# Kernel tuning notes

Measured on AMD Instinct MI355X. Metric: run time of the kernel, lower is better.

Reference implementation:

```python
import jax, jax.numpy as jnp
import numpy as np

B, N, E, H = 2, 4096, 1024, 16
HD = E // H                      # head_dim = 64
R = 8                            # LoRA rank
LORA_SCALE = 16.0 / R            # alpha / r = 2.0
BUCKET_SIZES = (256, 64, 16)


def setup_inputs() -> dict:
    key = jax.random.key(0)
    ks = jax.random.split(key, 24)
    inp = {"x": jax.random.normal(ks[0], (B, N, E), jnp.float32)}
    inp["wb_coarse"] = jax.random.randint(ks[1], (B, N), 0, 16)
    inp["wb_mid"] = jax.random.randint(ks[2], (B, N), 0, 64)
    inp["wb_fine"] = jax.random.randint(ks[3], (B, N), 0, 256)
    i = 4
    for name in ("q", "k", "v", "o"):
        inp[f"W{name}"] = jax.random.normal(ks[i], (E, E), jnp.float32) / np.sqrt(E); i += 1
        inp[f"b{name}"] = jax.random.normal(ks[i], (E,), jnp.float32) * 0.01; i += 1
        inp[f"A{name}"] = jax.random.normal(ks[i], (R, E), jnp.float32) / np.sqrt(E); i += 1
        inp[f"B{name}"] = jax.random.normal(ks[i], (E, R), jnp.float32) * 0.01; i += 1
    return inp


def _lora(x, W, b, A, Bm):
    # F.linear(x, W, b) + scale * x @ A.T @ B.T   (dropout=0 in eval)
    return x @ W.T + b + LORA_SCALE * ((x @ A.T) @ Bm.T)


def _chunked_attn(q, k, v, bidx, C):
    # q,k,v: [BH, N, D]; bidx: [BH, N] int; C: chunk size (divides N)
    BH, Nn, D = q.shape
    sidx = jnp.argsort(bidx, axis=1)
    uidx = jnp.argsort(sidx, axis=1)
    g = lambda t, i: jnp.take_along_axis(t, i[..., None], axis=1)
    qs, ks_, vs = g(q, sidx), g(k, sidx), g(v, sidx)
    nc = Nn // C
    qs = qs.reshape(BH, nc, C, D)
    ks_ = ks_.reshape(BH, nc, C, D)
    vs = vs.reshape(BH, nc, C, D)
    # previous chunk (look-back of one chunk); chunk 0 has no previous -> masked
    k_prev = jnp.concatenate([jnp.zeros_like(ks_[:, :1]), ks_[:, :-1]], axis=1)
    v_prev = jnp.concatenate([jnp.zeros_like(vs[:, :1]), vs[:, :-1]], axis=1)
    k_cat = jnp.concatenate([k_prev, ks_], axis=2)   # [BH, nc, 2C, D]
    v_cat = jnp.concatenate([v_prev, vs], axis=2)
    scores = jnp.einsum('bncd,bnkd->bnck', qs, k_cat) / jnp.sqrt(jnp.asarray(D, qs.dtype))
    # mask look-back keys for chunk 0 (torch path attends only within chunk 0)
    chunk_ids = jnp.arange(nc)[:, None, None]        # [nc,1,1]
    key_pos = jnp.arange(2 * C)[None, None, :]       # [1,1,2C]
    neg = jnp.finfo(scores.dtype).min
    scores = jnp.where((chunk_ids == 0) & (key_pos < C), neg, scores)
    attn = jax.nn.softmax(scores, axis=-1)
    out = jnp.einsum('bnck,bnkd->bncd', attn, v_cat).reshape(BH, Nn, D)
    return jnp.take_along_axis(out, uidx[..., None], axis=1)


def reference(x, wb_coarse, wb_mid, wb_fine,
              Wq, bq, Aq, Bq, Wk, bk, Ak, Bk,
              Wv, bv, Av, Bv, Wo, bo, Ao, Bo):
    q = _lora(x, Wq, bq, Aq, Bq)
    k = _lora(x, Wk, bk, Ak, Bk)
    v = _lora(x, Wv, bv, Av, Bv)
    to_heads = lambda t: t.reshape(B, N, H, HD).transpose(0, 2, 1, 3).reshape(B * H, N, HD)
    qh, kh, vh = to_heads(q), to_heads(k), to_heads(v)
    expand = lambda w: jnp.broadcast_to(w[:, None, :], (B, H, N)).reshape(B * H, N)
    wbs = (expand(wb_coarse), expand(wb_mid), expand(wb_fine))
    outs = (_chunked_attn(qh, kh, vh, wbs[0], BUCKET_SIZES[0])
            + _chunked_attn(qh, kh, vh, wbs[1], BUCKET_SIZES[1])
            + _chunked_attn(qh, kh, vh, wbs[2], BUCKET_SIZES[2])) / 3.0
    outs = outs.reshape(B, H, N, HD).transpose(0, 2, 1, 3).reshape(B, N, E)
    return _lora(outs, Wo, bo, Ao, Bo)
```

## Files before the change

kernel.cpp:

```cpp
#include <hip/hip_runtime.h>
#include <cstdint>
#include <cstddef>

#define BDIM 2
#define NTOK 4096
#define EDIM 1024
#define HEADS 16
#define HDIM 64
#define MROWS (BDIM * NTOK)

typedef unsigned short u16;
typedef __attribute__((ext_vector_type(8))) short bf16x8;
typedef __attribute__((ext_vector_type(8))) unsigned short u16x8;
typedef __attribute__((ext_vector_type(4))) float f32x4;

#define MFMA(a, b, c) __builtin_amdgcn_mfma_f32_16x16x32_bf16(a, b, c, 0, 0, 0)
#define BAR() asm volatile("s_barrier" ::: "memory")
#define SETPRIO(p) __builtin_amdgcn_s_setprio(p)

__device__ inline void split2(float x, u16& h, u16& l) {
    union { float f; unsigned u; } a;
    a.f = x;
    unsigned uh = a.u + 0x7fff + ((a.u >> 16) & 1);
    h = (u16)(uh >> 16);
// ... 34 lines not shown
    int o = idx >> 10, i = idx & 1023;
    float sum = 0.f;
#pragma unroll
    for (int r = 0; r < 8; ++r) sum += Bm[o * 8 + r] * A[r * 1024 + i];
    float w = W[idx] + 2.0f * sum;
    u16 h, l;
    split2(w, h, l);
    dh[idx] = h; dl[idx] = l;
}

__global__ __launch_bounds__(256) void split_kernel(
    const float* __restrict__ src, u16* __restrict__ dh, u16* __restrict__ dl)
{
    int idx = blockIdx.x * 256 + threadIdx.x;
    float4 v = ((const float4*)src)[idx];
    ushort4 h, l;
    split2(v.x, h.x, l.x);
    split2(v.y, h.y, l.y);
    split2(v.z, h.z, l.z);
    split2(v.w, h.w, l.w);
    ((ushort4*)dh)[idx] = h;
    ((ushort4*)dl)[idx] = l;
}

__global__ __launch_bounds__(256) void sort3_kernel(
    const int* __restrict__ w0, const int* __restrict__ w1,
    const int* __restrict__ w2, int* __restrict__ sidx)
{
    __shared__ int sb[NTOK];
    __shared__ int cnt[32][256];
    __shared__ int gb[256];
    const int* srcs[3] = {w0, w1, w2};
    int t = threadIdx.x;
    const int* w = srcs[blockIdx.y] + blockIdx.x * NTOK;
    int* outp = sidx + ((int)blockIdx.y * BDIM + (int)blockIdx.x) * NTOK;

    for (int i = t; i < NTOK; i += 256) sb[i] = w[i];
    for (int i = t; i < 32 * 256; i += 256) ((int*)cnt)[i] = 0;
    __syncthreads();

    int g = t >> 3;
#pragma unroll
    for (int e = 0; e < 16; ++e)
        atomicAdd(&cnt[g][sb[g * 128 + (t & 7) + 8 * e]], 1);
    __syncthreads();

    int run = 0;
#pragma unroll
    for (int gg = 0; gg < 32; ++gg) {
        int c = cnt[gg][t];
        cnt[gg][t] = run;
        run += c;
    }
    gb[t] = run;
    __syncthreads();
    if (t == 0) {
        int acc = 0;
        for (int v = 0; v < 256; ++v) { int c = gb[v]; gb[v] = acc; acc += c; }
    }
    __syncthreads();
    for (int i = t; i < 32 * 256; i += 256) {
        int v = i & 255, gg = i >> 8;
        cnt[gg][v] += gb[v];
    }
    __syncthreads();

    if (t < 32) {
        int base = t * 128;
        for (int e = 0; e < 128; ++e) {
            int v = sb[base + e];
            int p = cnt[t][v]++;
            outp[p] = base + e;
        }
    }
}

__global__ __launch_bounds__(512, 2) void gemm_qk_kernel(
    const u16* __restrict__ Xh, const u16* __restrict__ Xl,
    const u16* __restrict__ Wh, const u16* __restrict__ Wl,
    const float* __restrict__ bq, const float* __restrict__ bk,
    u16* __restrict__ qh, u16* __restrict__ ql,
    u16* __restrict__ kh, u16* __restrict__ kl)
{
    __shared__ __align__(16) unsigned char smem[131072];
    u16* lds = (u16*)smem;
    const int PA_h = 0, PA_l = 8192, PB_h = 16384, PB_l = 24576;

    int t = threadIdx.x;
    int lane = t & 63, wave = t >> 6;
    int bid = blockIdx.x;
    int wg = (bid & 7) * 32 + (bid >> 3);
    int bx = wg & 7, by = wg >> 3;
    int m0 = by * 256, n0 = bx * 256;

    int lrow = lane & 15, lq = lane >> 4;
    size_t aoff = (size_t)(m0 + wave * 32 + lrow) * EDIM + lq * 8;
    size_t boff = (size_t)(n0 + wave * 32 + lrow) * EDIM + lq * 8;
    int slabA = wave * 2;
    int sA0 = (wave >> 2) * 8;
    int sB0 = (wave & 3) * 4;
    f32x4 acc[8][4] = {};

    {
        u16* b0 = lds;
        GLL(Xh + aoff,             b0 + PA_h + (slabA + 0) * 512);
        GLL(Xh + aoff + 16 * EDIM, b0 + PA_h + (slabA + 1) * 512);
        GLL(Xl + aoff,             b0 + PA_l + (slabA + 0) * 512);
        GLL(Xl + aoff + 16 * EDIM, b0 + PA_l + (slabA + 1) * 512);
        GLL(Wh + boff,             b0 + PB_h + (slabA + 0) * 512);
        GLL(Wh + boff + 16 * EDIM, b0 + PB_h + (slabA + 1) * 512);
        GLL(Wl + boff,             b0 + PB_l + (slabA + 0) * 512);
        GLL(Wl + boff + 16 * EDIM, b0 + PB_l + (slabA + 1) * 512);
    }
    asm volatile("s_waitcnt vmcnt(0)" ::: "memory");
    BAR();

    for (int t32 = 0; t32 < 32; ++t32) {
        u16* rb   = lds + (t32 & 1) * 32768;
        u16* wbuf = lds + ((t32 + 1) & 1) * 32768;
        bool pf = (t32 + 1) < 32;
        int kn = (t32 + 1) * 32;
        bf16x8 bhf[4], blf[4];
#pragma unroll
        for (int p = 0; p < 4; ++p) {
            if (p == 0) {
#pragma unroll
                for (int j = 0; j < 4; ++j) {
                    bhf[j] = *(const bf16x8*)(rb + PB_h + (sB0 + j) * 512 + lane * 8);
                    blf[j] = *(const bf16x8*)(rb + PB_l + (sB0 + j) * 512 + lane * 8);
                }
            }
            bf16x8 a0h = *(const bf16x8*)(rb + PA_h + (sA0 + 2 * p)     * 512 + lane * 8);
            bf16x8 a0l = *(const bf16x8*)(rb + PA_l + (sA0 + 2 * p)     * 512 + lane * 8);
            bf16x8 a1h = *(const bf16x8*)(rb + PA_h + (sA0 + 2 * p + 1) * 512 + lane * 8);
            bf16x8 a1l = *(const bf16x8*)(rb + PA_l + (sA0 + 2 * p + 1) * 512 + lane * 8);
            if (pf) {
                if (p == 0) {
                    GLL(Xh + aoff + kn,             wbuf + PA_h + (slabA + 0) * 512);
                    GLL(Xh + aoff + kn + 16 * EDIM, wbuf + PA_h + (slabA + 1) * 512);
                    GLL(Xl + aoff + kn,             wbuf + PA_l + (slabA + 0) * 512);
                } else if (p == 1) {
                    GLL(Xl + aoff + kn + 16 * EDIM, wbuf + PA_l + (slabA + 1) * 512);
                    GLL(Wh + boff + kn,             wbuf + PB_h + (slabA + 0) * 512);
                    GLL(Wh + boff + kn + 16 * EDIM, wbuf + PB_h + (slabA + 1) * 512);
                } else if (p == 2) {
                    GLL(Wl + boff + kn,             wbuf + PB_l + (slabA + 0) * 512);
                    GLL(Wl + boff + kn + 16 * EDIM, wbuf + PB_l + (slabA + 1) * 512);
                }
            }
            BAR();
            SETPRIO(1);
#pragma unroll
            for (int j = 0; j < 4; ++j) {
                acc[2 * p][j]     = MFMA(a0h, bhf[j], acc[2 * p][j]);
                acc[2 * p][j]     = MFMA(a0h, blf[j], acc[2 * p][j]);
                acc[2 * p][j]     = MFMA(a0l, bhf[j], acc[2 * p][j]);
                acc[2 * p + 1][j] = MFMA(a1h, bhf[j], acc[2 * p + 1][j]);
                acc[2 * p + 1][j] = MFMA(a1h, blf[j], acc[2 * p + 1][j]);
                acc[2 * p + 1][j] = MFMA(a1l, bhf[j], acc[2 * p + 1][j]);
            }
            SETPRIO(0);
            if (p == 3) asm volatile("s_waitcnt vmcnt(0)" ::: "memory");
            BAR();
        }
    }

    int proj = n0 >> 10;
    const float* bias = proj ? bk : bq;
    u16* oh = proj ? kh : qh;
    u16* ol = proj ? kl : ql;
    int wm = (wave >> 2) * 128, wn = (wave & 3) * 64;
    int q4 = lane >> 4, l16 = lane & 15;
    int cb = (n0 & 1023) + wn;
    float bj[4];
#pragma unroll
    for (int j = 0; j < 4; ++j) bj[j] = bias[cb + j * 16 + l16];
    float* repw = (float*)smem + wave * 2176;
    int r8 = lane >> 3, c8 = lane & 7;
#pragma unroll
    for (int g = 0; g < 4; ++g) {
#pragma unroll
        for (int ii = 0; ii < 2; ++ii)
#pragma unroll
            for (int j = 0; j < 4; ++j)
#pragma unroll
                for (int r = 0; r < 4; ++r)
                    repw[(ii * 16 + q4 * 4 + r) * 68 + j * 16 + l16] =
                        acc[g * 2 + ii][j][r] + bj[j];
#pragma unroll
        for (int rg = 0; rg < 4; ++rg) {
            int lr = rg * 8 + r8;
            float4 f0 = *(float4*)(repw + lr * 68 + c8 * 8);
            float4 f1 = *(float4*)(repw + lr * 68 + c8 * 8 + 4);
            float fa[8] = {f0.x, f0.y, f0.z, f0.w, f1.x, f1.y, f1.z, f1.w};
            size_t off = (size_t)(m0 + wm + g * 32 + lr) * EDIM + cb + c8 * 8;
            u16x8 hv, lv;
#pragma unroll
            for (int e = 0; e < 8; ++e) {
                float v = fa[e];
                if (proj == 0) v *= 0.125f;
                u16 hh, ll;
                split2(v, hh, ll);
                hv[e] = hh; lv[e] = ll;
            }
            *(u16x8*)(oh + off) = hv;
            *(u16x8*)(ol + off) = lv;
        }
    }
}

__global__ __launch_bounds__(512, 2) void gemm_v_kernel(
    const u16* __restrict__ Xh, const u16* __restrict__ Wv,
    const float* __restrict__ bv, u16* __restrict__ vh)
{
    __shared__ __align__(16) unsigned char smem[73728];
    u16* lds = (u16*)smem;

    int t = threadIdx.x;
    int lane = t & 63, wave = t >> 6;
    int bid = blockIdx.x;
    int wg = (bid & 7) * 32 + (bid >> 3);
    int bx = wg & 7, by = wg >> 3;
    int m0 = by * 256, nc0 = bx * 128;

    int lrow = lane & 15, lq = lane >> 4;
    size_t aoff = (size_t)(m0 + wave * 32 + lrow) * EDIM + lq * 8;
    size_t boff = (size_t)(nc0 + wave * 16 + lrow) * EDIM + lq * 8;
    int slabA = wave * 2;
    int sA0 = (wave >> 1) * 4;
    int sB0 = (wave & 1) * 4;
    f32x4 acc[4][4] = {};

#pragma unroll
    for (int tt = 0; tt < 2; ++tt) {
        u16* sb = lds + tt * 12288;
        int kk = tt * 32;
        GLL(Xh + aoff + kk,             sb + (slabA + 0) * 512);
        GLL(Xh + aoff + kk + 16 * EDIM, sb + (slabA + 1) * 512);
        GLL(Wv + boff + kk,             sb + 8192 + wave * 512);
    }
    asm volatile("s_waitcnt vmcnt(3)" ::: "memory");
    BAR();

    for (int t32 = 0; t32 < 32; ++t32) {
        u16* rb = lds + (t32 % 3) * 12288;
        u16* sb = lds + ((t32 + 2) % 3) * 12288;
        bool pf = (t32 + 2) < 32;
        int kn = (t32 + 2) * 32;

        bf16x8 bhf[4];
#pragma unroll
        for (int j = 0; j < 4; ++j)
            bhf[j] = *(const bf16x8*)(rb + 8192 + (sB0 + j) * 512 + lane * 8);
        bf16x8 a0 = *(const bf16x8*)(rb + (sA0 + 0) * 512 + lane * 8);
        bf16x8 a1 = *(const bf16x8*)(rb + (sA0 + 1) * 512 + lane * 8);
        if (pf) {
            GLL(Xh + aoff + kn,             sb + (slabA + 0) * 512);
            GLL(Xh + aoff + kn + 16 * EDIM, sb + (slabA + 1) * 512);
        }
        BAR();
        SETPRIO(1);
#pragma unroll
        for (int j = 0; j < 4; ++j) {
            acc[0][j] = MFMA(a0, bhf[j], acc[0][j]);
            acc[1][j] = MFMA(a1, bhf[j], acc[1][j]);
        }
        SETPRIO(0);
        BAR();

        bf16x8 a2 = *(const bf16x8*)(rb + (sA0 + 2) * 512 + lane * 8);
        bf16x8 a3 = *(const bf16x8*)(rb + (sA0 + 3) * 512 + lane * 8);
        if (pf) GLL(Wv + boff + kn, sb + 8192 + wave * 512);
        BAR();
        SETPRIO(1);
#pragma unroll
        for (int j = 0; j < 4; ++j) {
            acc[2][j] = MFMA(a2, bhf[j], acc[2][j]);
            acc[3][j] = MFMA(a3, bhf[j], acc[3][j]);
        }
        SETPRIO(0);
        if (pf) asm volatile("s_waitcnt vmcnt(3)" ::: "memory");
        else    asm volatile("s_waitcnt vmcnt(0)" ::: "memory");
        BAR();
    }

    int wm = (wave >> 1) * 64, wn = (wave & 1) * 64;
    int q4 = lane >> 4, l16 = lane & 15;
    int cb = nc0 + wn;
    float bj[4];
#pragma unroll
    for (int j = 0; j < 4; ++j) bj[j] = bv[cb + j * 16 + l16];
    float* repw = (float*)smem + wave * 2176;
    int r8 = lane >> 3, c8 = lane & 7;
#pragma unroll
    for (int g = 0; g < 2; ++g) {
#pragma unroll
        for (int ii = 0; ii < 2; ++ii)
#pragma unroll
            for (int j = 0; j < 4; ++j)
#pragma unroll
                for (int r = 0; r < 4; ++r)
                    repw[(ii * 16 + q4 * 4 + r) * 68 + j * 16 + l16] =
                        acc[g * 2 + ii][j][r] + bj[j];
#pragma unroll
        for (int rg = 0; rg < 4; ++rg) {
            int lr = rg * 8 + r8;
            float4 f0 = *(float4*)(repw + lr * 68 + c8 * 8);
            float4 f1 = *(float4*)(repw + lr * 68 + c8 * 8 + 4);
            float fa[8] = {f0.x, f0.y, f0.z, f0.w, f1.x, f1.y, f1.z, f1.w};
            size_t off = (size_t)(m0 + wm + g * 32 + lr) * EDIM + cb + c8 * 8;
            u16x8 hv;
#pragma unroll
            for (int e = 0; e < 8; ++e) hv[e] = bf16rne(fa[e]);
            *(u16x8*)(vh + off) = hv;
        }
    }
}

__global__ __launch_bounds__(512, 2) void gemm_o_kernel(
    const u16* __restrict__ Xh, const u16* __restrict__ Xl,
    const u16* __restrict__ Wh, const u16* __restrict__ Wl,
    const float* __restrict__ bias, float* __restrict__ Y)
{
    __shared__ __align__(16) unsigned char smem[147456];
    u16* lds = (u16*)smem;
    const int PA_h = 0, PA_l = 8192, PB_h = 16384, PB_l = 20480;

    int t = threadIdx.x;
    int lane = t & 63, wave = t >> 6;
    int bid = blockIdx.x;
    int wg = (bid & 7) * 32 + (bid >> 3);
    int bx = wg & 7, by = wg >> 3;
    int m0 = by * 256, n0 = bx * 128;

    int lrow = lane & 15, lq = lane >> 4;
    size_t aoff = (size_t)(m0 + wave * 32 + lrow) * EDIM + lq * 8;
    size_t boff = (size_t)(n0 + wave * 16 + lrow) * EDIM + lq * 8;
    int slabA = wave * 2;
    int sA0 = (wave >> 1) * 4;
    int sB0 = (wave & 1) * 4;
    f32x4 acc[4][4] = {};

#pragma unroll
    for (int tt = 0; tt < 2; ++tt) {
        u16* sb = lds + tt * 24576;
        int kk = tt * 32;
        GLL(Xh + aoff + kk,             sb + PA_h + (slabA + 0) * 512);
        GLL(Xh + aoff + kk + 16 * EDIM, sb + PA_h + (slabA + 1) * 512);
        GLL(Xl + aoff + kk,             sb + PA_l + (slabA + 0) * 512);
        GLL(Xl + aoff + kk + 16 * EDIM, sb + PA_l + (slabA + 1) * 512);
        GLL(Wh + boff + kk,             sb + PB_h + wave * 512);
        GLL(Wl + boff + kk,             sb + PB_l + wave * 512);
    }
    asm volatile("s_waitcnt vmcnt(6)" ::: "memory");
    BAR();

    for (int t32 = 0; t32 < 32; ++t32) {
        u16* rb = lds + (t32 % 3) * 24576;
        u16* sb = lds + ((t32 + 2) % 3) * 24576;
        bool pf = (t32 + 2) < 32;
        int kn = (t32 + 2) * 32;
        bf16x8 bhf[4], blf[4];
#pragma unroll
        for (int p = 0; p < 4; ++p) {
            if (p == 0) {
#pragma unroll
                for (int j = 0; j < 4; ++j) {
                    bhf[j] = *(const bf16x8*)(rb + PB_h + (sB0 + j) * 512 + lane * 8);
                    blf[j] = *(const bf16x8*)(rb + PB_l + (sB0 + j) * 512 + lane * 8);
                }
            }
            bf16x8 aph = *(const bf16x8*)(rb + PA_h + (sA0 + p) * 512 + lane * 8);
            bf16x8 apl = *(const bf16x8*)(rb + PA_l + (sA0 + p) * 512 + lane * 8);
            if (pf) {
                if (p == 0) {
                    GLL(Xh + aoff + kn,             sb + PA_h + (slabA + 0) * 512);
                    GLL(Xh + aoff + kn + 16 * EDIM, sb + PA_h + (slabA + 1) * 512);
                } else if (p == 1) {
                    GLL(Xl + aoff + kn,             sb + PA_l + (slabA + 0) * 512);
                    GLL(Xl + aoff + kn + 16 * EDIM, sb + PA_l + (slabA + 1) * 512);
                } else if (p == 2) {
                    GLL(Wh + boff + kn, sb + PB_h + wave * 512);
                    GLL(Wl + boff + kn, sb + PB_l + wave * 512);
                }
            }
            BAR();
            SETPRIO(1);
#pragma unroll
            for (int j = 0; j < 4; ++j) {
                acc[p][j] = MFMA(aph, bhf[j], acc[p][j]);
                acc[p][j] = MFMA(aph, blf[j], acc[p][j]);
                acc[p][j] = MFMA(apl, bhf[j], acc[p][j]);
            }
            SETPRIO(0);
            if (p == 3) {
                if (pf) asm volatile("s_waitcnt vmcnt(6)" ::: "memory");
                else    asm volatile("s_waitcnt vmcnt(0)" ::: "memory");
            }
            BAR();
        }
    }

    int wm = (wave >> 1) * 64, wn = (wave & 1) * 64;
    int col_in = lane & 15, rquad = lane >> 4;
#pragma unroll
    for (int j = 0; j < 4; ++j) {
        int col = n0 + wn + j * 16 + col_in;
        float bvv = bias[col];
#pragma unroll
        for (int i = 0; i < 4; ++i) {
            int mbase = m0 + wm + i * 16 + rquad * 4;
#pragma unroll
            for (int r = 0; r < 4; ++r)
                Y[(size_t)(mbase + r) * EDIM + col] = acc[i][j][r] + bvv;
        }
    }
}

template <int C>
__global__ __launch_bounds__(256, 3) void attn_mfma_kernel(
    const u16* __restrict__ Qh, const u16* __restrict__ Ql,
    const u16* __restrict__ Kh, const u16* __restrict__ Kl,
    const u16* __restrict__ Vh, const int* __restrict__ sidx,
    float* __restrict__ out)
{
    __shared__ u16 KfH[4096], KfL[4096];
    __shared__ u16 VL[64 * 72];
    __shared__ u16 PbH[4 * 16 * 56];

    int t = threadIdx.x;
    int lane = t & 63, wave = t >> 6;
    int quad = lane >> 4, l16 = lane & 15;
    int bh = blockIdx.y, b = bh >> 4, h = bh & 15;
    int p0 = blockIdx.x * 128;
    const int* sxb = sidx + b * NTOK;

    int ptile[2], ws_[2], we_[2];
    bf16x8 qhf[2][2], qlf[2][2];
#pragma unroll
    for (int tq = 0; tq < 2; ++tq) {
        ptile[tq] = p0 + wave * 32 + tq * 16;
        int c = ptile[tq] / C;
        ws_[tq] = (c > 0) ? (c - 1) * C : 0;
        we_[tq] = (c + 1) * C;
        int qrow = sxb[ptile[tq] + l16];
        size_t rb = (size_t)(b * NTOK + qrow) * EDIM + h * HDIM + quad * 8;
#pragma unroll
        for (int kk = 0; kk < 2; ++kk) {
            qhf[tq][kk] = *(const bf16x8*)(Qh + rb + kk * 32);
            qlf[tq][kk] = *(const bf16x8*)(Ql + rb + kk * 32);
        }
    }

    f32x4 oacc[2][4] = {};
    float lpart[2][4] = {};
    float mrun[2] = {-1e30f, -1e30f};

    int c0 = p0 / C, c1 = (p0 + 127) / C;
    int kmin = (c0 > 0) ? (c0 - 1) * C : 0;
    int kmax = (c1 + 1) * C;

    for (int ks = kmin; ks < kmax; ks += 64) {
        int nk = min(64, kmax - ks);
        __syncthreads();

        {
            int key16 = lane & 15, qd = lane >> 4;
            int tok = sxb[min(ks + wave * 16 + key16, NTOK - 1)];
            size_t rb = (size_t)(b * NTOK + tok) * EDIM + h * HDIM + qd * 8;
            GLL(Kh + rb,      KfH + (wave * 2 + 0) * 512);
            GLL(Kh + rb + 32, KfH + (wave * 2 + 1) * 512);
            GLL(Kl + rb,      KfL + (wave * 2 + 0) * 512);
            GLL(Kl + rb + 32, KfL + (wave * 2 + 1) * 512);
        }
#pragma unroll
        for (int it = 0; it < 2; ++it) {
            int c = it * 256 + t;
            int key = c & 63, dg = c >> 6;
            int tok = sxb[min(ks + key, NTOK - 1)];
            bf16x8 vv = *(const bf16x8*)(Vh + (size_t)(b * NTOK + tok) * EDIM + h * HDIM + dg * 8);
#pragma unroll
            for (int e = 0; e < 8; ++e)
                VL[(dg * 8 + e) * 72 + key] = (u16)vv[e];
        }
        __syncthreads();

        int jlo0 = max(ks, ws_[0]) - ks, jhi0 = min(ks + nk, we_[0]) - ks;
        int jlo1 = max(ks, ws_[1]) - ks, jhi1 = min(ks + nk, we_[1]) - ks;
        bool e0 = jlo0 < jhi0, e1 = jlo1 < jhi1;
        if (!e0 && !e1) continue;
        int glo = e0 ? (e1 ? min(jlo0, jlo1) : jlo0) : jlo1;
        int ghi = e0 ? (e1 ? max(jhi0, jhi1) : jhi0) : jhi1;

        for (int g0 = glo & ~31; g0 < ghi; g0 += 32) {
            int s0i = g0 >> 4;
            int s1i = min(s0i + 1, 3);
            bf16x8 kh0[2], kl0[2], kh1[2], kl1[2];
#pragma unroll
            for (int kk = 0; kk < 2; ++kk) {
                kh0[kk] = *(const bf16x8*)(KfH + ((s0i * 2 + kk) * 64 + lane) * 8);
                kl0[kk] = *(const bf16x8*)(KfL + ((s0i * 2 + kk) * 64 + lane) * 8);
                kh1[kk] = *(const bf16x8*)(KfH + ((s1i * 2 + kk) * 64 + lane) * 8);
                kl1[kk] = *(const bf16x8*)(KfL + ((s1i * 2 + kk) * 64 + lane) * 8);
            }
#pragma unroll
            for (int tq = 0; tq < 2; ++tq) {
                int jl = tq ? jlo1 : jlo0, jh = tq ? jhi1 : jhi0;
                bool v0 = (g0 >= jl) && (g0 < jh);
                bool v1 = (g0 + 16 >= jl) && (g0 + 16 < jh);
                if (!v0 && !v1) continue;
                f32x4 sa = {0.f, 0.f, 0.f, 0.f}, sb2 = {0.f, 0.f, 0.f, 0.f};
                if (v0) {
                    sa = MFMA(qhf[tq][0], kh0[0], sa);
                    sa = MFMA(qhf[tq][0], kl0[0], sa);
                    sa = MFMA(qlf[tq][0], kh0[0], sa);
                    sa = MFMA(qhf[tq][1], kh0[1], sa);
                    sa = MFMA(qhf[tq][1], kl0[1], sa);
                    sa = MFMA(qlf[tq][1], kh0[1], sa);
                }
                if (v1) {
                    sb2 = MFMA(qhf[tq][0], kh1[0], sb2);
                    sb2 = MFMA(qhf[tq][0], kl1[0], sb2);
                    sb2 = MFMA(qlf[tq][0], kh1[0], sb2);
                    sb2 = MFMA(qhf[tq][1], kh1[1], sb2);
                    sb2 = MFMA(qhf[tq][1], kl1[1], sb2);
                    sb2 = MFMA(qlf[tq][1], kh1[1], sb2);
                }
                float smax = -1e30f;
                if (v0) smax = fmaxf(smax, fmaxf(fmaxf(sa[0], sa[1]), fmaxf(sa[2], sa[3])));
                if (v1) smax = fmaxf(smax, fmaxf(fmaxf(sb2[0], sb2[1]), fmaxf(sb2[2], sb2[3])));
                smax = fmaxf(smax, __shfl_xor(smax, 1));
                smax = fmaxf(smax, __shfl_xor(smax, 2));
                smax = fmaxf(smax, __shfl_xor(smax, 4));
                smax = fmaxf(smax, __shfl_xor(smax, 8));
                float mold = mrun[tq];
                float mnew = fmaxf(mold, smax);
                mrun[tq] = mnew;
                float alpha = __expf(mold - mnew);
#pragma unroll
                for (int r = 0; r < 4; ++r) lpart[tq][r] *= alpha;
#pragma unroll
                for (int dt = 0; dt < 4; ++dt) {
                    oacc[tq][dt][0] *= alpha; oacc[tq][dt][1] *= alpha;
                    oacc[tq][dt][2] *= alpha; oacc[tq][dt][3] *= alpha;
                }
                u16* pbh = PbH + wave * 896;
#pragma unroll
                for (int r = 0; r < 4; ++r) {
                    float pa = v0 ? __expf(sa[r] - mnew) : 0.f;
                    float pb = v1 ? __expf(sb2[r] - mnew) : 0.f;
                    lpart[tq][r] += pa + pb;
                    pbh[(quad * 4 + r) * 56 + l16] = bf16rne(pa);
                    pbh[(quad * 4 + r) * 56 + 16 + l16] = bf16rne(pb);
                }
                bf16x8 ph = *(const bf16x8*)(pbh + l16 * 56 + quad * 8);
                int kh2 = g0 >> 5;
#pragma unroll
                for (int dt = 0; dt < 4; ++dt) {
                    bf16x8 vv = *(const bf16x8*)(VL + (dt * 16 + l16) * 72 + kh2 * 32 + quad * 8);
                    oacc[tq][dt] = MFMA(ph, vv, oacc[tq][dt]);
                }
            }
        }
    }

#pragma unroll
    for (int tq = 0; tq < 2; ++tq) {
        float inv[4];
#pragma unroll
        for (int r = 0; r < 4; ++r) {
            float v = lpart[tq][r];
            v += __shfl_xor(v, 1);
            v += __shfl_xor(v, 2);
            v += __shfl_xor(v, 4);
            v += __shfl_xor(v, 8);
            inv[r] = 1.0f / (3.0f * v);
        }
#pragma unroll
        for (int r = 0; r < 4; ++r) {
            int tok = sxb[ptile[tq] + quad * 4 + r];
            float* op = out + (size_t)(b * NTOK + tok) * EDIM + h * HDIM + l16;
#pragma unroll
            for (int dt = 0; dt < 4; ++dt)
                op[dt * 16] += oacc[tq][dt][r] * inv[r];
        }
    }
}

extern "C" void kernel_launch(void* const* d_in, const int* in_sizes, int n_in,
                              void* d_out, int out_size, void* d_ws, size_t ws_size,
                              hipStream_t stream)
{
    const float* x   = (const float*)d_in[0];
    const int*   wbc = (const int*)d_in[1];
    const int*   wbm = (const int*)d_in[2];
    const int*   wbf = (const int*)d_in[3];
    const float* Wq = (const float*)d_in[4],  *bq = (const float*)d_in[5];
    const float* Aq = (const float*)d_in[6],  *Bq = (const float*)d_in[7];
    const float* Wk = (const float*)d_in[8],  *bk = (const float*)d_in[9];
    const float* Ak = (const float*)d_in[10], *Bk = (const float*)d_in[11];
    const float* Wv = (const float*)d_in[12], *bv = (const float*)d_in[13];
    const float* Av = (const float*)d_in[14], *Bv = (const float*)d_in[15];
    const float* Wo = (const float*)d_in[16], *bo = (const float*)d_in[17];
    const float* Ao = (const float*)d_in[18], *Bo = (const float*)d_in[19];

    const size_t EE  = (size_t)EDIM * EDIM;
    const size_t BNE = (size_t)MROWS * EDIM;

    char* wsb = (char*)d_ws;
    float* ab = (float*)wsb;                        wsb += BNE * 4;
    u16* xh = (u16*)wsb;                            wsb += BNE * 2;
    u16* xl = (u16*)wsb;                            wsb += BNE * 2;
    u16* qh = (u16*)wsb;                            wsb += BNE * 2;
    u16* ql = (u16*)wsb;                            wsb += BNE * 2;
    u16* kh = (u16*)wsb;                            wsb += BNE * 2;
    u16* kl = (u16*)wsb;                            wsb += BNE * 2;
    u16* vh = (u16*)wsb;                            wsb += BNE * 2;
    u16* wh_all = (u16*)wsb;                        wsb += 3 * EE * 2;
    u16* wl_all = (u16*)wsb;                        wsb += 3 * EE * 2;
    u16* woh = (u16*)wsb;                           wsb += EE * 2;
    u16* wol = (u16*)wsb;                           wsb += EE * 2;
    int* sidx = (int*)wsb;                          wsb += 3 * BDIM * NTOK * 4;

    hipMemsetAsync(ab, 0, BNE * sizeof(float), stream);

    split_kernel<<<BNE / 1024, 256, 0, stream>>>(x, xh, xl);

    build_weff4_kernel<<<dim3(4096, 4), 256, 0, stream>>>(
        Wq, Aq, Bq, Wk, Ak, Bk, Wv, Av, Bv, Wo, Ao, Bo,
        wh_all + 0 * EE, wl_all + 0 * EE,
        wh_all + 1 * EE, wl_all + 1 * EE,
        wh_all + 2 * EE, wl_all + 2 * EE,
        woh, wol);

    sort3_kernel<<<dim3(BDIM, 3), 256, 0, stream>>>(wbc, wbm, wbf, sidx);

    gemm_qk_kernel<<<256, 512, 0, stream>>>(xh, xl, wh_all, wl_all,
                                            bq, bk, qh, ql, kh, kl);
    gemm_v_kernel<<<256, 512, 0, stream>>>(xh, wh_all + 2 * EE, bv, vh);

    dim3 ga(NTOK / 128, BDIM * HEADS);
    attn_mfma_kernel<256><<<ga, 256, 0, stream>>>(qh, ql, kh, kl, vh, sidx + 0 * BDIM * NTOK, ab);
    attn_mfma_kernel<64><<<ga, 256, 0, stream>>>(qh, ql, kh, kl, vh, sidx + 1 * BDIM * NTOK, ab);
    attn_mfma_kernel<16><<<ga, 256, 0, stream>>>(qh, ql, kh, kl, vh, sidx + 2 * BDIM * NTOK, ab);

    split_kernel<<<BNE / 1024, 256, 0, stream>>>(ab, xh, xl);
    gemm_o_kernel<<<256, 512, 0, stream>>>(xh, xl, woh, wol, bo, (float*)d_out);
}
```

Measured before the change: 511.7 us.

## Retile QK GEMM with triple buffering, prefetch attention K/V, fuse output split

The QK projection GEMM moves to 256x128 tiles with a three-stage LDS ring and 512 blocks, matching the layout of the other GEMMs. The attention kernel double-buffers K in LDS and prefetches V into registers for the next 64-key step, and only rescales the running max when the jump exceeds a threshold. The first attention pass writes its output instead of accumulating, which removes the memset. The last pass does the hi/lo bf16 split of the combined output itself, which removes the separate split kernel. These changes add LDS use and register pressure in exchange for less exposed load latency and fewer launches and memory passes.

```diff
diff --git a/kernel.cpp b/kernel.cpp
--- a/kernel.cpp
+++ b/kernel.cpp
@@ -140,44 +140,44 @@
     u16* __restrict__ qh, u16* __restrict__ ql,
     u16* __restrict__ kh, u16* __restrict__ kl)
 {
-    __shared__ __align__(16) unsigned char smem[131072];
+    __shared__ __align__(16) unsigned char smem[147456];
     u16* lds = (u16*)smem;
-    const int PA_h = 0, PA_l = 8192, PB_h = 16384, PB_l = 24576;
+    const int PA_h = 0, PA_l = 8192, PB_h = 16384, PB_l = 20480;
 
     int t = threadIdx.x;
     int lane = t & 63, wave = t >> 6;
     int bid = blockIdx.x;
-    int wg = (bid & 7) * 32 + (bid >> 3);
-    int bx = wg & 7, by = wg >> 3;
-    int m0 = by * 256, n0 = bx * 256;
+    int wg = (bid & 7) * 64 + (bid >> 3);
+    int bx = wg & 15, by = wg >> 4;
+    int m0 = by * 256, n0 = bx * 128;
 
     int lrow = lane & 15, lq = lane >> 4;
     size_t aoff = (size_t)(m0 + wave * 32 + lrow) * EDIM + lq * 8;
-    size_t boff = (size_t)(n0 + wave * 32 + lrow) * EDIM + lq * 8;
+    size_t boff = (size_t)(n0 + wave * 16 + lrow) * EDIM + lq * 8;
     int slabA = wave * 2;
-    int sA0 = (wave >> 2) * 8;
-    int sB0 = (wave & 3) * 4;
-    f32x4 acc[8][4] = {};
-
-    {
-        u16* b0 = lds;
-        GLL(Xh + aoff,             b0 + PA_h + (slabA + 0) * 512);
-        GLL(Xh + aoff + 16 * EDIM, b0 + PA_h + (slabA + 1) * 512);
-        GLL(Xl + aoff,             b0 + PA_l + (slabA + 0) * 512);
-        GLL(Xl + aoff + 16 * EDIM, b0 + PA_l + (slabA + 1) * 512);
-        GLL(Wh + boff,             b0 + PB_h + (slabA + 0) * 512);
-        GLL(Wh + boff + 16 * EDIM, b0 + PB_h + (slabA + 1) * 512);
-        GLL(Wl + boff,             b0 + PB_l + (slabA + 0) * 512);
-        GLL(Wl + boff + 16 * EDIM, b0 + PB_l + (slabA + 1) * 512);
-    }
-    asm volatile("s_waitcnt vmcnt(0)" ::: "memory");
+    int sA0 = (wave >> 1) * 4;
+    int sB0 = (wave & 1) * 4;
+    f32x4 acc[4][4] = {};
+
+#pragma unroll
+    for (int tt = 0; tt < 2; ++tt) {
+        u16* sbuf = lds + tt * 24576;
+        int kk = tt * 32;
+        GLL(Xh + aoff + kk,             sbuf + PA_h + (slabA + 0) * 512);
+        GLL(Xh + aoff + kk + 16 * EDIM, sbuf + PA_h + (slabA + 1) * 512);
+        GLL(Xl + aoff + kk,             sbuf + PA_l + (slabA + 0) * 512);
+        GLL(Xl + aoff + kk + 16 * EDIM, sbuf + PA_l + (slabA + 1) * 512);
+        GLL(Wh + boff + kk, sbuf + PB_h + wave * 512);
+        GLL(Wl + boff + kk, sbuf + PB_l + wave * 512);
+    }
+    asm volatile("s_waitcnt vmcnt(6)" ::: "memory");
     BAR();
 
     for (int t32 = 0; t32 < 32; ++t32) {
-        u16* rb   = lds + (t32 & 1) * 32768;
-        u16* wbuf = lds + ((t32 + 1) & 1) * 32768;
-        bool pf = (t32 + 1) < 32;
-        int kn = (t32 + 1) * 32;
+        u16* rb = lds + (t32 % 3) * 24576;
+        u16* sbuf = lds + ((t32 + 2) % 3) * 24576;
+        bool pf = (t32 + 2) < 32;
+        int kn = (t32 + 2) * 32;
         bf16x8 bhf[4], blf[4];
 #pragma unroll
         for (int p = 0; p < 4; ++p) {
@@ -188,46 +188,42 @@
                     blf[j] = *(const bf16x8*)(rb + PB_l + (sB0 + j) * 512 + lane * 8);
                 }
             }
-            bf16x8 a0h = *(const bf16x8*)(rb + PA_h + (sA0 + 2 * p)     * 512 + lane * 8);
-            bf16x8 a0l = *(const bf16x8*)(rb + PA_l + (sA0 + 2 * p)     * 512 + lane * 8);
-            bf16x8 a1h = *(const bf16x8*)(rb + PA_h + (sA0 + 2 * p + 1) * 512 + lane * 8);
-            bf16x8 a1l = *(const bf16x8*)(rb + PA_l + (sA0 + 2 * p + 1) * 512 + lane * 8);
+            bf16x8 aph = *(const bf16x8*)(rb + PA_h + (sA0 + p) * 512 + lane * 8);
+            bf16x8 apl = *(const bf16x8*)(rb + PA_l + (sA0 + p) * 512 + lane * 8);
             if (pf) {
                 if (p == 0) {
-                    GLL(Xh + aoff + kn,             wbuf + PA_h + (slabA + 0) * 512);
-                    GLL(Xh + aoff + kn + 16 * EDIM, wbuf + PA_h + (slabA + 1) * 512);
-                    GLL(Xl + aoff + kn,             wbuf + PA_l + (slabA + 0) * 512);
+                    GLL(Xh + aoff + kn,             sbuf + PA_h + (slabA + 0) * 512);
+                    GLL(Xh + aoff + kn + 16 * EDIM, sbuf + PA_h + (slabA + 1) * 512);
                 } else if (p == 1) {
-                    GLL(Xl + aoff + kn + 16 * EDIM, wbuf + PA_l + (slabA + 1) * 512);
-                    GLL(Wh + boff + kn,             wbuf + PB_h + (slabA + 0) * 512);
-                    GLL(Wh + boff + kn + 16 * EDIM, wbuf + PB_h + (slabA + 1) * 512);
+                    GLL(Xl + aoff + kn,             sbuf + PA_l + (slabA + 0) * 512);
+                    GLL(Xl + aoff + kn + 16 * EDIM, sbuf + PA_l + (slabA + 1) * 512);
                 } else if (p == 2) {
-                    GLL(Wl + boff + kn,             wbuf + PB_l + (slabA + 0) * 512);
-                    GLL(Wl + boff + kn + 16 * EDIM, wbuf + PB_l + (slabA + 1) * 512);
+                    GLL(Wh + boff + kn, sbuf + PB_h + wave * 512);
+                    GLL(Wl + boff + kn, sbuf + PB_l + wave * 512);
                 }
             }
             BAR();
             SETPRIO(1);
 #pragma unroll
             for (int j = 0; j < 4; ++j) {
-                acc[2 * p][j]     = MFMA(a0h, bhf[j], acc[2 * p][j]);
-                acc[2 * p][j]     = MFMA(a0h, blf[j], acc[2 * p][j]);
-                acc[2 * p][j]     = MFMA(a0l, bhf[j], acc[2 * p][j]);
-                acc[2 * p + 1][j] = MFMA(a1h, bhf[j], acc[2 * p + 1][j]);
-                acc[2 * p + 1][j] = MFMA(a1h, blf[j], acc[2 * p + 1][j]);
-                acc[2 * p + 1][j] = MFMA(a1l, bhf[j], acc[2 * p + 1][j]);
+                acc[p][j] = MFMA(aph, bhf[j], acc[p][j]);
+                acc[p][j] = MFMA(aph, blf[j], acc[p][j]);
+                acc[p][j] = MFMA(apl, bhf[j], acc[p][j]);
             }
             SETPRIO(0);
-            if (p == 3) asm volatile("s_waitcnt vmcnt(0)" ::: "memory");
+            if (p == 3) {
+                if (pf) asm volatile("s_waitcnt vmcnt(6)" ::: "memory");
+                else    asm volatile("s_waitcnt vmcnt(0)" ::: "memory");
+            }
             BAR();
         }
     }
 
     int proj = n0 >> 10;
     const float* bias = proj ? bk : bq;
-    u16* oh = proj ? kh : qh;
-    u16* ol = proj ? kl : ql;
-    int wm = (wave >> 2) * 128, wn = (wave & 3) * 64;
+    u16* ohp = proj ? kh : qh;
+    u16* olp = proj ? kl : ql;
+    int wm = (wave >> 1) * 64, wn = (wave & 1) * 64;
     int q4 = lane >> 4, l16 = lane & 15;
     int cb = (n0 & 1023) + wn;
     float bj[4];
@@ -236,7 +232,7 @@
     float* repw = (float*)smem + wave * 2176;
     int r8 = lane >> 3, c8 = lane & 7;
 #pragma unroll
-    for (int g = 0; g < 4; ++g) {
+    for (int gph = 0; gph < 2; ++gph) {
 #pragma unroll
         for (int ii = 0; ii < 2; ++ii)
 #pragma unroll
@@ -244,14 +240,14 @@
 #pragma unroll
                 for (int r = 0; r < 4; ++r)
                     repw[(ii * 16 + q4 * 4 + r) * 68 + j * 16 + l16] =
-                        acc[g * 2 + ii][j][r] + bj[j];
+                        acc[gph * 2 + ii][j][r] + bj[j];
 #pragma unroll
         for (int rg = 0; rg < 4; ++rg) {
             int lr = rg * 8 + r8;
             float4 f0 = *(float4*)(repw + lr * 68 + c8 * 8);
             float4 f1 = *(float4*)(repw + lr * 68 + c8 * 8 + 4);
             float fa[8] = {f0.x, f0.y, f0.z, f0.w, f1.x, f1.y, f1.z, f1.w};
-            size_t off = (size_t)(m0 + wm + g * 32 + lr) * EDIM + cb + c8 * 8;
+            size_t off = (size_t)(m0 + wm + gph * 32 + lr) * EDIM + cb + c8 * 8;
             u16x8 hv, lv;
 #pragma unroll
             for (int e = 0; e < 8; ++e) {
@@ -261,8 +257,8 @@
                 split2(v, hh, ll);
                 hv[e] = hh; lv[e] = ll;
             }
-            *(u16x8*)(oh + off) = hv;
-            *(u16x8*)(ol + off) = lv;
+            *(u16x8*)(ohp + off) = hv;
+            *(u16x8*)(olp + off) = lv;
         }
     }
 }
@@ -291,18 +287,18 @@
 
 #pragma unroll
     for (int tt = 0; tt < 2; ++tt) {
-        u16* sb = lds + tt * 12288;
+        u16* sbuf = lds + tt * 12288;
         int kk = tt * 32;
-        GLL(Xh + aoff + kk,             sb + (slabA + 0) * 512);
-        GLL(Xh + aoff + kk + 16 * EDIM, sb + (slabA + 1) * 512);
-        GLL(Wv + boff + kk,             sb + 8192 + wave * 512);
+        GLL(Xh + aoff + kk,             sbuf + (slabA + 0) * 512);
+        GLL(Xh + aoff + kk + 16 * EDIM, sbuf + (slabA + 1) * 512);
+        GLL(Wv + boff + kk,             sbuf + 8192 + wave * 512);
     }
     asm volatile("s_waitcnt vmcnt(3)" ::: "memory");
     BAR();
 
     for (int t32 = 0; t32 < 32; ++t32) {
         u16* rb = lds + (t32 % 3) * 12288;
-        u16* sb = lds + ((t32 + 2) % 3) * 12288;
+        u16* sbuf = lds + ((t32 + 2) % 3) * 12288;
         bool pf = (t32 + 2) < 32;
         int kn = (t32 + 2) * 32;
 
@@ -313,8 +309,8 @@
         bf16x8 a0 = *(const bf16x8*)(rb + (sA0 + 0) * 512 + lane * 8);
         bf16x8 a1 = *(const bf16x8*)(rb + (sA0 + 1) * 512 + lane * 8);
         if (pf) {
-            GLL(Xh + aoff + kn,             sb + (slabA + 0) * 512);
-            GLL(Xh + aoff + kn + 16 * EDIM, sb + (slabA + 1) * 512);
+            GLL(Xh + aoff + kn,             sbuf + (slabA + 0) * 512);
+            GLL(Xh + aoff + kn + 16 * EDIM, sbuf + (slabA + 1) * 512);
         }
         BAR();
         SETPRIO(1);
@@ -328,7 +324,7 @@
 
         bf16x8 a2 = *(const bf16x8*)(rb + (sA0 + 2) * 512 + lane * 8);
         bf16x8 a3 = *(const bf16x8*)(rb + (sA0 + 3) * 512 + lane * 8);
-        if (pf) GLL(Wv + boff + kn, sb + 8192 + wave * 512);
+        if (pf) GLL(Wv + boff + kn, sbuf + 8192 + wave * 512);
         BAR();
         SETPRIO(1);
 #pragma unroll
@@ -351,7 +347,7 @@
     float* repw = (float*)smem + wave * 2176;
     int r8 = lane >> 3, c8 = lane & 7;
 #pragma unroll
-    for (int g = 0; g < 2; ++g) {
+    for (int gph = 0; gph < 2; ++gph) {
 #pragma unroll
         for (int ii = 0; ii < 2; ++ii)
 #pragma unroll
@@ -359,14 +355,14 @@
 #pragma unroll
                 for (int r = 0; r < 4; ++r)
                     repw[(ii * 16 + q4 * 4 + r) * 68 + j * 16 + l16] =
-                        acc[g * 2 + ii][j][r] + bj[j];
+                        acc[gph * 2 + ii][j][r] + bj[j];
 #pragma unroll
         for (int rg = 0; rg < 4; ++rg) {
             int lr = rg * 8 + r8;
             float4 f0 = *(float4*)(repw + lr * 68 + c8 * 8);
             float4 f1 = *(float4*)(repw + lr * 68 + c8 * 8 + 4);
             float fa[8] = {f0.x, f0.y, f0.z, f0.w, f1.x, f1.y, f1.z, f1.w};
-            size_t off = (size_t)(m0 + wm + g * 32 + lr) * EDIM + cb + c8 * 8;
+            size_t off = (size_t)(m0 + wm + gph * 32 + lr) * EDIM + cb + c8 * 8;
             u16x8 hv;
 #pragma unroll
             for (int e = 0; e < 8; ++e) hv[e] = bf16rne(fa[e]);
@@ -401,21 +397,21 @@
 
 #pragma unroll
     for (int tt = 0; tt < 2; ++tt) {
-        u16* sb = lds + tt * 24576;
+        u16* sbuf = lds + tt * 24576;
         int kk = tt * 32;
-        GLL(Xh + aoff + kk,             sb + PA_h + (slabA + 0) * 512);
-        GLL(Xh + aoff + kk + 16 * EDIM, sb + PA_h + (slabA + 1) * 512);
-        GLL(Xl + aoff + kk,             sb + PA_l + (slabA + 0) * 512);
-        GLL(Xl + aoff + kk + 16 * EDIM, sb + PA_l + (slabA + 1) * 512);
-        GLL(Wh + boff + kk,             sb + PB_h + wave * 512);
-        GLL(Wl + boff + kk,             sb + PB_l + wave * 512);
+        GLL(Xh + aoff + kk,             sbuf + PA_h + (slabA + 0) * 512);
+        GLL(Xh + aoff + kk + 16 * EDIM, sbuf + PA_h + (slabA + 1) * 512);
+        GLL(Xl + aoff + kk,             sbuf + PA_l + (slabA + 0) * 512);
+        GLL(Xl + aoff + kk + 16 * EDIM, sbuf + PA_l + (slabA + 1) * 512);
+        GLL(Wh + boff + kk, sbuf + PB_h + wave * 512);
+        GLL(Wl + boff + kk, sbuf + PB_l + wave * 512);
     }
     asm volatile("s_waitcnt vmcnt(6)" ::: "memory");
     BAR();
 
     for (int t32 = 0; t32 < 32; ++t32) {
         u16* rb = lds + (t32 % 3) * 24576;
-        u16* sb = lds + ((t32 + 2) % 3) * 24576;
+        u16* sbuf = lds + ((t32 + 2) % 3) * 24576;
         bool pf = (t32 + 2) < 32;
         int kn = (t32 + 2) * 32;
         bf16x8 bhf[4], blf[4];
@@ -432,14 +428,14 @@
             bf16x8 apl = *(const bf16x8*)(rb + PA_l + (sA0 + p) * 512 + lane * 8);
             if (pf) {
                 if (p == 0) {
-                    GLL(Xh + aoff + kn,             sb + PA_h + (slabA + 0) * 512);
-                    GLL(Xh + aoff + kn + 16 * EDIM, sb + PA_h + (slabA + 1) * 512);
+                    GLL(Xh + aoff + kn,             sbuf + PA_h + (slabA + 0) * 512);
+                    GLL(Xh + aoff + kn + 16 * EDIM, sbuf + PA_h + (slabA + 1) * 512);
                 } else if (p == 1) {
-                    GLL(Xl + aoff + kn,             sb + PA_l + (slabA + 0) * 512);
-                    GLL(Xl + aoff + kn + 16 * EDIM, sb + PA_l + (slabA + 1) * 512);
+                    GLL(Xl + aoff + kn,             sbuf + PA_l + (slabA + 0) * 512);
+                    GLL(Xl + aoff + kn + 16 * EDIM, sbuf + PA_l + (slabA + 1) * 512);
                 } else if (p == 2) {
-                    GLL(Wh + boff + kn, sb + PB_h + wave * 512);
-                    GLL(Wl + boff + kn, sb + PB_l + wave * 512);
+                    GLL(Wh + boff + kn, sbuf + PB_h + wave * 512);
+                    GLL(Wl + boff + kn, sbuf + PB_l + wave * 512);
                 }
             }
             BAR();
@@ -475,14 +471,14 @@
     }
 }
 
-template <int C>
+template <int C, bool ACC, bool OSPLIT>
 __global__ __launch_bounds__(256, 3) void attn_mfma_kernel(
     const u16* __restrict__ Qh, const u16* __restrict__ Ql,
     const u16* __restrict__ Kh, const u16* __restrict__ Kl,
     const u16* __restrict__ Vh, const int* __restrict__ sidx,
-    float* __restrict__ out)
+    float* __restrict__ out, u16* __restrict__ osh, u16* __restrict__ osl)
 {
-    __shared__ u16 KfH[4096], KfL[4096];
+    __shared__ u16 KfH[2][4096], KfL[2][4096];
     __shared__ u16 VL[64 * 72];
     __shared__ u16 PbH[4 * 16 * 56];
 
@@ -517,109 +513,156 @@
     int c0 = p0 / C, c1 = (p0 + 127) / C;
     int kmin = (c0 > 0) ? (c0 - 1) * C : 0;
     int kmax = (c1 + 1) * C;
-
-    for (int ks = kmin; ks < kmax; ks += 64) {
-        int nk = min(64, kmax - ks);
-        __syncthreads();
-
-        {
-            int key16 = lane & 15, qd = lane >> 4;
-            int tok = sxb[min(ks + wave * 16 + key16, NTOK - 1)];
-            size_t rb = (size_t)(b * NTOK + tok) * EDIM + h * HDIM + qd * 8;
-            GLL(Kh + rb,      KfH + (wave * 2 + 0) * 512);
-            GLL(Kh + rb + 32, KfH + (wave * 2 + 1) * 512);
-            GLL(Kl + rb,      KfL + (wave * 2 + 0) * 512);
-            GLL(Kl + rb + 32, KfL + (wave * 2 + 1) * 512);
-        }
+    int nsteps = (kmax - kmin + 63) >> 6;
+
+    {
+        int tok = sxb[min(kmin + wave * 16 + l16, NTOK - 1)];
+        size_t rb = (size_t)(b * NTOK + tok) * EDIM + h * HDIM + quad * 8;
+        GLL(Kh + rb,      &KfH[0][(wave * 2 + 0) * 512]);
+        GLL(Kh + rb + 32, &KfH[0][(wave * 2 + 1) * 512]);
+        GLL(Kl + rb,      &KfL[0][(wave * 2 + 0) * 512]);
+        GLL(Kl + rb + 32, &KfL[0][(wave * 2 + 1) * 512]);
+        bf16x8 vreg[2];
 #pragma unroll
         for (int it = 0; it < 2; ++it) {
             int c = it * 256 + t;
             int key = c & 63, dg = c >> 6;
-            int tok = sxb[min(ks + key, NTOK - 1)];
-            bf16x8 vv = *(const bf16x8*)(Vh + (size_t)(b * NTOK + tok) * EDIM + h * HDIM + dg * 8);
+            int tok2 = sxb[min(kmin + key, NTOK - 1)];
+            vreg[it] = *(const bf16x8*)(Vh + (size_t)(b * NTOK + tok2) * EDIM + h * HDIM + dg * 8);
+        }
+#pragma unroll
+        for (int it = 0; it < 2; ++it) {
+            int c = it * 256 + t;
+            int key = c & 63, dg = c >> 6;
 #pragma unroll
             for (int e = 0; e < 8; ++e)
-                VL[(dg * 8 + e) * 72 + key] = (u16)vv[e];
-        }
+                VL[(dg * 8 + e) * 72 + key] = (u16)vreg[it][e];
+        }
+        asm volatile("s_waitcnt vmcnt(0)" ::: "memory");
         __syncthreads();
+    }
+
+    int pb = 0;
+    for (int s = 0; s < nsteps; ++s) {
+        int ks = kmin + s * 64;
+        int nk = min(64, kmax - ks);
+        bool pf = (s + 1) < nsteps;
+        bf16x8 vreg[2];
+        if (pf) {
+            int ks2 = ks + 64;
+            int tok = sxb[min(ks2 + wave * 16 + l16, NTOK - 1)];
+            size_t rb = (size_t)(b * NTOK + tok) * EDIM + h * HDIM + quad * 8;
+            GLL(Kh + rb,      &KfH[pb ^ 1][(wave * 2 + 0) * 512]);
+            GLL(Kh + rb + 32, &KfH[pb ^ 1][(wave * 2 + 1) * 512]);
+            GLL(Kl + rb,      &KfL[pb ^ 1][(wave * 2 + 0) * 512]);
+            GLL(Kl + rb + 32, &KfL[pb ^ 1][(wave * 2 + 1) * 512]);
+#pragma unroll
+            for (int it = 0; it < 2; ++it) {
+                int c = it * 256 + t;
+                int key = c & 63, dg = c >> 6;
+                int tok2 = sxb[min(ks2 + key, NTOK - 1)];
+                vreg[it] = *(const bf16x8*)(Vh + (size_t)(b * NTOK + tok2) * EDIM + h * HDIM + dg * 8);
+            }
+        }
 
         int jlo0 = max(ks, ws_[0]) - ks, jhi0 = min(ks + nk, we_[0]) - ks;
         int jlo1 = max(ks, ws_[1]) - ks, jhi1 = min(ks + nk, we_[1]) - ks;
         bool e0 = jlo0 < jhi0, e1 = jlo1 < jhi1;
-        if (!e0 && !e1) continue;
-        int glo = e0 ? (e1 ? min(jlo0, jlo1) : jlo0) : jlo1;
-        int ghi = e0 ? (e1 ? max(jhi0, jhi1) : jhi0) : jhi1;
-
-        for (int g0 = glo & ~31; g0 < ghi; g0 += 32) {
-            int s0i = g0 >> 4;
-            int s1i = min(s0i + 1, 3);
-            bf16x8 kh0[2], kl0[2], kh1[2], kl1[2];
-#pragma unroll
-            for (int kk = 0; kk < 2; ++kk) {
-                kh0[kk] = *(const bf16x8*)(KfH + ((s0i * 2 + kk) * 64 + lane) * 8);
-                kl0[kk] = *(const bf16x8*)(KfL + ((s0i * 2 + kk) * 64 + lane) * 8);
-                kh1[kk] = *(const bf16x8*)(KfH + ((s1i * 2 + kk) * 64 + lane) * 8);
-                kl1[kk] = *(const bf16x8*)(KfL + ((s1i * 2 + kk) * 64 + lane) * 8);
-            }
-#pragma unroll
-            for (int tq = 0; tq < 2; ++tq) {
-                int jl = tq ? jlo1 : jlo0, jh = tq ? jhi1 : jhi0;
-                bool v0 = (g0 >= jl) && (g0 < jh);
-                bool v1 = (g0 + 16 >= jl) && (g0 + 16 < jh);
-                if (!v0 && !v1) continue;
-                f32x4 sa = {0.f, 0.f, 0.f, 0.f}, sb2 = {0.f, 0.f, 0.f, 0.f};
-                if (v0) {
-                    sa = MFMA(qhf[tq][0], kh0[0], sa);
-                    sa = MFMA(qhf[tq][0], kl0[0], sa);
-                    sa = MFMA(qlf[tq][0], kh0[0], sa);
-                    sa = MFMA(qhf[tq][1], kh0[1], sa);
-                    sa = MFMA(qhf[tq][1], kl0[1], sa);
-                    sa = MFMA(qlf[tq][1], kh0[1], sa);
+        if (e0 || e1) {
+            int glo = e0 ? (e1 ? min(jlo0, jlo1) : jlo0) : jlo1;
+            int ghi = e0 ? (e1 ? max(jhi0, jhi1) : jhi0) : jhi1;
+            const u16* kfh = &KfH[pb][0];
+            const u16* kfl = &KfL[pb][0];
+
+            for (int g0 = glo & ~31; g0 < ghi; g0 += 32) {
+                int s0i = g0 >> 4;
+                int s1i = min(s0i + 1, 3);
+                bf16x8 kh0[2], kl0[2], kh1[2], kl1[2];
+#pragma unroll
+                for (int kk = 0; kk < 2; ++kk) {
+                    kh0[kk] = *(const bf16x8*)(kfh + ((s0i * 2 + kk) * 64 + lane) * 8);
+                    kl0[kk] = *(const bf16x8*)(kfl + ((s0i * 2 + kk) * 64 + lane) * 8);
+                    kh1[kk] = *(const bf16x8*)(kfh + ((s1i * 2 + kk) * 64 + lane) * 8);
+                    kl1[kk] = *(const bf16x8*)(kfl + ((s1i * 2 + kk) * 64 + lane) * 8);
                 }
-                if (v1) {
-                    sb2 = MFMA(qhf[tq][0], kh1[0], sb2);
-                    sb2 = MFMA(qhf[tq][0], kl1[0], sb2);
-                    sb2 = MFMA(qlf[tq][0], kh1[0], sb2);
-                    sb2 = MFMA(qhf[tq][1], kh1[1], sb2);
-                    sb2 = MFMA(qhf[tq][1], kl1[1], sb2);
-                    sb2 = MFMA(qlf[tq][1], kh1[1], sb2);
+#pragma unroll
+                for (int tq = 0; tq < 2; ++tq) {
+                    int jl = tq ? jlo1 : jlo0, jh = tq ? jhi1 : jhi0;
+                    bool v0 = (g0 >= jl) && (g0 < jh);
+                    bool v1 = (g0 + 16 >= jl) && (g0 + 16 < jh);
+                    if (!v0 && !v1) continue;
+                    f32x4 sa = {0.f, 0.f, 0.f, 0.f}, sb2 = {0.f, 0.f, 0.f, 0.f};
+                    if (v0) {
+                        sa = MFMA(qhf[tq][0], kh0[0], sa);
+                        sa = MFMA(qhf[tq][0], kl0[0], sa);
+                        sa = MFMA(qlf[tq][0], kh0[0], sa);
+                        sa = MFMA(qhf[tq][1], kh0[1], sa);
+                        sa = MFMA(qhf[tq][1], kl0[1], sa);
+                        sa = MFMA(qlf[tq][1], kh0[1], sa);
+                    }
+                    if (v1) {
+                        sb2 = MFMA(qhf[tq][0], kh1[0], sb2);
+                        sb2 = MFMA(qhf[tq][0], kl1[0], sb2);
+                        sb2 = MFMA(qlf[tq][0], kh1[0], sb2);
+                        sb2 = MFMA(qhf[tq][1], kh1[1], sb2);
+                        sb2 = MFMA(qhf[tq][1], kl1[1], sb2);
+                        sb2 = MFMA(qlf[tq][1], kh1[1], sb2);
+                    }
+                    float smax = -1e30f;
+                    if (v0) smax = fmaxf(smax, fmaxf(fmaxf(sa[0], sa[1]), fmaxf(sa[2], sa[3])));
+                    if (v1) smax = fmaxf(smax, fmaxf(fmaxf(sb2[0], sb2[1]), fmaxf(sb2[2], sb2[3])));
+                    smax = fmaxf(smax, __shfl_xor(smax, 1));
+                    smax = fmaxf(smax, __shfl_xor(smax, 2));
+                    smax = fmaxf(smax, __shfl_xor(smax, 4));
+                    smax = fmaxf(smax, __shfl_xor(smax, 8));
+                    float mold = mrun[tq];
+                    float mnew = mold;
+                    if (smax > mold + 8.0f) {
+                        mnew = smax;
+                        mrun[tq] = mnew;
+                        float alpha = __expf(mold - mnew);
+#pragma unroll
+                        for (int r = 0; r < 4; ++r) lpart[tq][r] *= alpha;
+#pragma unroll
+                        for (int dt = 0; dt < 4; ++dt) {
+                            oacc[tq][dt][0] *= alpha; oacc[tq][dt][1] *= alpha;
+                            oacc[tq][dt][2] *= alpha; oacc[tq][dt][3] *= alpha;
+                        }
+                    }
+                    u16* pbh = PbH + wave * 896;
+#pragma unroll
+                    for (int r = 0; r < 4; ++r) {
+                        float pa = v0 ? __expf(sa[r] - mnew) : 0.f;
+                        float pbv = v1 ? __expf(sb2[r] - mnew) : 0.f;
+                        lpart[tq][r] += pa + pbv;
+                        pbh[(quad * 4 + r) * 56 + l16] = bf16rne(pa);
+                        pbh[(quad * 4 + r) * 56 + 16 + l16] = bf16rne(pbv);
+                    }
+                    bf16x8 ph = *(const bf16x8*)(pbh + l16 * 56 + quad * 8);
+                    int kh2 = g0 >> 5;
+#pragma unroll
+                    for (int dt = 0; dt < 4; ++dt) {
+                        bf16x8 vv = *(const bf16x8*)(VL + (dt * 16 + l16) * 72 + kh2 * 32 + quad * 8);
+                        oacc[tq][dt] = MFMA(ph, vv, oacc[tq][dt]);
+                    }
                 }
-                float smax = -1e30f;
-                if (v0) smax = fmaxf(smax, fmaxf(fmaxf(sa[0], sa[1]), fmaxf(sa[2], sa[3])));
-                if (v1) smax = fmaxf(smax, fmaxf(fmaxf(sb2[0], sb2[1]), fmaxf(sb2[2], sb2[3])));
-                smax = fmaxf(smax, __shfl_xor(smax, 1));
-                smax = fmaxf(smax, __shfl_xor(smax, 2));
-                smax = fmaxf(smax, __shfl_xor(smax, 4));
-                smax = fmaxf(smax, __shfl_xor(smax, 8));
-                float mold = mrun[tq];
-                float mnew = fmaxf(mold, smax);
-                mrun[tq] = mnew;
-                float alpha = __expf(mold - mnew);
-#pragma unroll
-                for (int r = 0; r < 4; ++r) lpart[tq][r] *= alpha;
-#pragma unroll
-                for (int dt = 0; dt < 4; ++dt) {
-                    oacc[tq][dt][0] *= alpha; oacc[tq][dt][1] *= alpha;
-                    oacc[tq][dt][2] *= alpha; oacc[tq][dt][3] *= alpha;
-                }
-                u16* pbh = PbH + wave * 896;
-#pragma unroll
-                for (int r = 0; r < 4; ++r) {
-                    float pa = v0 ? __expf(sa[r] - mnew) : 0.f;
-                    float pb = v1 ? __expf(sb2[r] - mnew) : 0.f;
-                    lpart[tq][r] += pa + pb;
-                    pbh[(quad * 4 + r) * 56 + l16] = bf16rne(pa);
-                    pbh[(quad * 4 + r) * 56 + 16 + l16] = bf16rne(pb);
-                }
-                bf16x8 ph = *(const bf16x8*)(pbh + l16 * 56 + quad * 8);
-                int kh2 = g0 >> 5;
-#pragma unroll
-                for (int dt = 0; dt < 4; ++dt) {
-                    bf16x8 vv = *(const bf16x8*)(VL + (dt * 16 + l16) * 72 + kh2 * 32 + quad * 8);
-                    oacc[tq][dt] = MFMA(ph, vv, oacc[tq][dt]);
-                }
-            }
-        }
+            }
+        }
+
+        asm volatile("s_waitcnt vmcnt(0)" ::: "memory");
+        __syncthreads();
+        if (pf) {
+#pragma unroll
+            for (int it = 0; it < 2; ++it) {
+                int c = it * 256 + t;
+                int key = c & 63, dg = c >> 6;
+#pragma unroll
+                for (int e = 0; e < 8; ++e)
+                    VL[(dg * 8 + e) * 72 + key] = (u16)vreg[it][e];
+            }
+        }
+        __syncthreads();
+        pb ^= 1;
     }
 
 #pragma unroll
@@ -637,10 +680,25 @@
 #pragma unroll
         for (int r = 0; r < 4; ++r) {
             int tok = sxb[ptile[tq] + quad * 4 + r];
-            float* op = out + (size_t)(b * NTOK + tok) * EDIM + h * HDIM + l16;
-#pragma unroll
-            for (int dt = 0; dt < 4; ++dt)
-                op[dt * 16] += oacc[tq][dt][r] * inv[r];
+            size_t base = (size_t)(b * NTOK + tok) * EDIM + h * HDIM + l16;
+            if (OSPLIT) {
+#pragma unroll
+                for (int dt = 0; dt < 4; ++dt) {
+                    float v = out[base + dt * 16] + oacc[tq][dt][r] * inv[r];
+                    u16 hh, ll;
+                    split2(v, hh, ll);
+                    osh[base + dt * 16] = hh;
+                    osl[base + dt * 16] = ll;
+                }
+            } else if (ACC) {
+#pragma unroll
+                for (int dt = 0; dt < 4; ++dt)
+                    out[base + dt * 16] += oacc[tq][dt][r] * inv[r];
+            } else {
+#pragma unroll
+                for (int dt = 0; dt < 4; ++dt)
+                    out[base + dt * 16] = oacc[tq][dt][r] * inv[r];
+            }
         }
     }
 }
@@ -680,8 +738,6 @@
     u16* wol = (u16*)wsb;                           wsb += EE * 2;
     int* sidx = (int*)wsb;                          wsb += 3 * BDIM * NTOK * 4;
 
-    hipMemsetAsync(ab, 0, BNE * sizeof(float), stream);
-
     split_kernel<<<BNE / 1024, 256, 0, stream>>>(x, xh, xl);
 
     build_weff4_kernel<<<dim3(4096, 4), 256, 0, stream>>>(
@@ -693,15 +749,17 @@
 
     sort3_kernel<<<dim3(BDIM, 3), 256, 0, stream>>>(wbc, wbm, wbf, sidx);
 
-    gemm_qk_kernel<<<256, 512, 0, stream>>>(xh, xl, wh_all, wl_all,
+    gemm_qk_kernel<<<512, 512, 0, stream>>>(xh, xl, wh_all, wl_all,
                                             bq, bk, qh, ql, kh, kl);
     gemm_v_kernel<<<256, 512, 0, stream>>>(xh, wh_all + 2 * EE, bv, vh);
 
     dim3 ga(NTOK / 128, BDIM * HEADS);
-    attn_mfma_kernel<256><<<ga, 256, 0, stream>>>(qh, ql, kh, kl, vh, sidx + 0 * BDIM * NTOK, ab);
-    attn_mfma_kernel<64><<<ga, 256, 0, stream>>>(qh, ql, kh, kl, vh, sidx + 1 * BDIM * NTOK, ab);
-    attn_mfma_kernel<16><<<ga, 256, 0, stream>>>(qh, ql, kh, kl, vh, sidx + 2 * BDIM * NTOK, ab);
-
-    split_kernel<<<BNE / 1024, 256, 0, stream>>>(ab, xh, xl);
+    attn_mfma_kernel<256, false, false><<<ga, 256, 0, stream>>>(
+        qh, ql, kh, kl, vh, sidx + 0 * BDIM * NTOK, ab, xh, xl);
+    attn_mfma_kernel<64, true, false><<<ga, 256, 0, stream>>>(
+        qh, ql, kh, kl, vh, sidx + 1 * BDIM * NTOK, ab, xh, xl);
+    attn_mfma_kernel<16, true, true><<<ga, 256, 0, stream>>>(
+        qh, ql, kh, kl, vh, sidx + 2 * BDIM * NTOK, ab, xh, xl);
+
     gemm_o_kernel<<<256, 512, 0, stream>>>(xh, xl, woh, wol, bo, (float*)d_out);
 }
```

Result: no change. 510.0 us (-0.3%).
